# Performance work log

Hardware: AMD Instinct MI355X
Metric: run time of the kernel (lower is better)

## Reference

```python
import jax, jax.numpy as jnp
import numpy as np

B, N, D_MODEL, H, FF = 8, 1024, 1024, 16, 4096
HEAD_DIM = D_MODEL // H
SCALE = float(np.sqrt(HEAD_DIM))


def layer_norm(x, g, b, eps=1e-5):
    mu = jnp.mean(x, axis=-1, keepdims=True)
    var = jnp.var(x, axis=-1, keepdims=True)
    return (x - mu) * jax.lax.rsqrt(var + eps) * g + b


def setup_inputs() -> dict:
    key = jax.random.key(0)
    ks = jax.random.split(key, 16)
    s = lambda fan_in: 1.0 / np.sqrt(fan_in)
    return {
        "hidden_states": jax.random.normal(ks[0], (B, N, D_MODEL), jnp.float32),
        "attention_mask": jnp.zeros((B, N), dtype=bool),
        "qkv_w": jax.random.uniform(ks[1], (3 * D_MODEL, D_MODEL), jnp.float32, -s(D_MODEL), s(D_MODEL)),
        "qkv_b": jnp.zeros((3 * D_MODEL,), jnp.float32),
        "out_w": jax.random.uniform(ks[2], (D_MODEL, D_MODEL), jnp.float32, -s(D_MODEL), s(D_MODEL)),
        "out_b": jnp.zeros((D_MODEL,), jnp.float32),
        "query_weights": jax.random.normal(ks[3], (H, D_MODEL), jnp.float32) * 0.04,  # xavier-ish
        "key_weights": jax.random.normal(ks[4], (H, D_MODEL), jnp.float32) * 0.04,
        "norm1_g": jnp.ones((D_MODEL,), jnp.float32),
        "norm1_b": jnp.zeros((D_MODEL,), jnp.float32),
        "norm2_g": jnp.ones((D_MODEL,), jnp.float32),
        "norm2_b": jnp.zeros((D_MODEL,), jnp.float32),
        "lin1_w": jax.random.uniform(ks[5], (FF, D_MODEL), jnp.float32, -s(D_MODEL), s(D_MODEL)),
        "lin1_b": jnp.zeros((FF,), jnp.float32),
        "lin2_w": jax.random.uniform(ks[6], (D_MODEL, FF // 2), jnp.float32, -s(FF // 2), s(FF // 2)),
        "lin2_b": jnp.zeros((D_MODEL,), jnp.float32),
    }


def reference(hidden_states, attention_mask, qkv_w, qkv_b, out_w, out_b,
              query_weights, key_weights, norm1_g, norm1_b, norm2_g, norm2_b,
              lin1_w, lin1_b, lin2_w, lin2_b):
    b, n, c = hidden_states.shape
    h = layer_norm(hidden_states, norm1_g, norm1_b)
    qkv = (h @ qkv_w.T + qkv_b).reshape(b, n, 3, H, c // H)
    qkv = jnp.transpose(qkv, (2, 0, 3, 1, 4))  # [3, B, H, N, D]
    q, k, v = qkv[0], qkv[1], qkv[2]
    mask4 = attention_mask[:, None, :, None]  # [B,1,N,1]

    # additive attention on keys: per-(head, position) scalar weight, softmax over N
    # (note: original also computes a global_query from q, but it is unused downstream)
    key_attn = k * key_weights[None, :, :, None] / SCALE  # einsum 'bhnd,hn->bhnd'
    key_attn = jnp.where(mask4, -1e9, key_attn)
    key_weight = jax.nn.softmax(key_attn, axis=2)
    global_key = jnp.sum(key_weight * k, axis=2, keepdims=True)  # [B,H,1,D]

    out = v * global_key  # broadcast over N
    out = jnp.transpose(out, (0, 2, 1, 3)).reshape(b, n, c)
    out = out @ out_w.T + out_b
    hidden_states = hidden_states + out

    h2 = layer_norm(hidden_states, norm2_g, norm2_b)
    ff = h2 @ lin1_w.T + lin1_b
    a, g = jnp.split(ff, 2, axis=-1)
    ff = (a * jax.nn.relu(g)) @ lin2_w.T + lin2_b
    return hidden_states + ff
```

## Files before the change

kernel.cpp:

```cpp
#include <hip/hip_runtime.h>
#include <math.h>


#define DM     1024
#define FFH    2048
#define M_TOT  8192

typedef _Float16 f16x8 __attribute__((ext_vector_type(8)));
typedef float    f32x4 __attribute__((ext_vector_type(4)));

__device__ __forceinline__ void gl2lds16(const void* g, void* l) {
    __builtin_amdgcn_global_load_lds(
        (const __attribute__((address_space(1))) void*)g,
        (__attribute__((address_space(3))) void*)l, 16, 0, 0);
}
__device__ __forceinline__ unsigned short f2h(float x) {
    union { _Float16 h; unsigned short u; } c;
    c.h = (_Float16)x;
    return c.u;
}

__global__ __launch_bounds__(256) void wcast_all(
    const float* __restrict__ s0, const float* __restrict__ s1,
    const float* __restrict__ s2, const float* __restrict__ s3,
    unsigned short* __restrict__ d0, unsigned short* __restrict__ d1,
    unsigned short* __restrict__ d2, unsigned short* __restrict__ d3)
{
    const int i = blockIdx.x * 256 + threadIdx.x;
    const float* s; unsigned short* d; int off;
    if      (i <  524288) { s = s0; d = d0; off = i; }
    else if (i <  786432) { s = s1; d = d1; off = i - 524288; }
    else if (i < 1835008) { s = s2; d = d2; off = i - 786432; }
    else                  { s = s3; d = d3; off = i - 1835008; }
    const float4 v = ((const float4*)s)[off];
    ushort4 h;
    h.x = f2h(v.x); h.y = f2h(v.y); h.z = f2h(v.z); h.w = f2h(v.w);
    ((ushort4*)d)[off] = h;
}

__global__ __launch_bounds__(256) void ln_f16(
    const float* __restrict__ x, const float* __restrict__ g,
    const float* __restrict__ b, unsigned short* __restrict__ y)
{
    const int row = blockIdx.x;
    const int t   = threadIdx.x;
    const float4 v = ((const float4*)(x + (size_t)row * DM))[t];

    float s  = v.x + v.y + v.z + v.w;
    float ss = v.x * v.x + v.y * v.y + v.z * v.z + v.w * v.w;
    #pragma unroll
    for (int off = 32; off > 0; off >>= 1) {
        s  += __shfl_xor(s, off);
        ss += __shfl_xor(ss, off);
    }
    __shared__ float sm[8];
    const int wave = t >> 6;
    if ((t & 63) == 0) { sm[wave * 2] = s; sm[wave * 2 + 1] = ss; }
    __syncthreads();
    s  = sm[0] + sm[2] + sm[4] + sm[6];
    ss = sm[1] + sm[3] + sm[5] + sm[7];

    const float mu  = s * (1.0f / DM);
    const float var = ss * (1.0f / DM) - mu * mu;
    const float r   = rsqrtf(var + 1e-5f);

    const float4 gv = ((const float4*)g)[t];
    const float4 bv = ((const float4*)b)[t];
    ushort4 o;
    o.x = f2h((v.x - mu) * r * gv.x + bv.x);
    o.y = f2h((v.y - mu) * r * gv.y + bv.y);
    o.z = f2h((v.z - mu) * r * gv.z + bv.z);
    o.w = f2h((v.w - mu) * r * gv.w + bv.w);
    ((ushort4*)(y + (size_t)row * DM))[t] = o;
}

__global__ __launch_bounds__(256) void attn_kernel(
    const float* __restrict__ kv, const float* __restrict__ kw,
    float* __restrict__ gk)
{
    const int bh = blockIdx.x;
    const int b  = bh >> 4;
    const int h  = bh & 15;
    const int t  = threadIdx.x;
    const int e  = t & 63;
    const int w  = t >> 6;

    const float* kbase = kv + (size_t)b * 1024 * 2048 + h * 64 + e;
    const float* kwr   = kw + h * 1024;

    float m = -1e30f, l = 0.0f, s = 0.0f;
    #pragma unroll 4
    for (int i = 0; i < 256; ++i) {
        const int   n    = (w << 8) + i;
        const float kval = kbase[(size_t)n * 2048];
        const float x    = kval * kwr[n] * 0.125f;
        const float nm   = fmaxf(m, x);
        const float corr = __expf(m - nm);
        const float ex   = __expf(x - nm);
        l = l * corr + ex;
        s = s * corr + ex * kval;
        m = nm;
    }
    __shared__ float sm[3][256];
    sm[0][t] = m; sm[1][t] = l; sm[2][t] = s;
    __syncthreads();
    if (t < 64) {
        #pragma unroll
        for (int ww = 1; ww < 4; ++ww) {
            const float m2 = sm[0][ww * 64 + e];
            const float l2 = sm[1][ww * 64 + e];
            const float s2 = sm[2][ww * 64 + e];
            const float nm = fmaxf(m, m2);
            const float c1 = __expf(m - nm);
            const float c2 = __expf(m2 - nm);
            l = l * c1 + l2 * c2;
            s = s * c1 + s2 * c2;
            m = nm;
        }
        gk[(size_t)b * DM + h * 64 + e] = s / l;
    }
}

__global__ __launch_bounds__(256) void vscale_f16(
    const float* __restrict__ kv, const float* __restrict__ gk,
    unsigned short* __restrict__ vq)
{
    const int m = blockIdx.x;
    const int t = threadIdx.x;
    const int b = m >> 10;
    const float4 v = *(const float4*)(kv + (size_t)m * 2048 + 1024 + t * 4);
    const float4 s = *(const float4*)(gk + b * DM + t * 4);
    ushort4 o;
    o.x = f2h(v.x * s.x);
    o.y = f2h(v.y * s.y);
    o.z = f2h(v.z * s.z);
    o.w = f2h(v.w * s.w);
    *(ushort4*)(vq + (size_t)m * DM + t * 4) = o;
}

template <bool LIN1ACT, bool HAS_RES>
__global__ __launch_bounds__(256) void mfma_gemm(
    const unsigned short* __restrict__ A,
    const unsigned short* __restrict__ B,
    const float* __restrict__ bias,
    const float* __restrict__ residual,
    float* __restrict__ Cf,
    unsigned short* __restrict__ Cq,
    int K, int lda, int ldc)
{
    __shared__ char lds[32768];
    char* ldsA = lds;
    char* ldsB = lds + 16384;

    const int t  = threadIdx.x;
    const int m0 = blockIdx.y * 128;
    const int n0 = blockIdx.x * (LIN1ACT ? 64 : 128);
    const int L  = t & 63;
    const int w  = t >> 6;
    const int wm = w >> 1, wn = w & 1;
    const int fr = L & 15;
    const int q  = L >> 4;

    const unsigned short* Br0 = B + (size_t)n0 * K;
    const unsigned short* Br1 = B + (size_t)(FFH + n0) * K;

    f32x4 acc[4][4];
    #pragma unroll
    for (int i = 0; i < 4; ++i)
        #pragma unroll
        for (int j = 0; j < 4; ++j) acc[i][j] = (f32x4){0.f, 0.f, 0.f, 0.f};

    for (int k0 = 0; k0 < K; k0 += 64) {
        __syncthreads();
        #pragma unroll
        for (int j = 0; j < 4; ++j) {
            const int c   = t + j * 256;
            const int row = c >> 3;
            const int ch  = (c & 7) ^ (row & 7);
            gl2lds16(A + (size_t)(m0 + row) * lda + k0 + ch * 8,
                     ldsA + c * 16);
        }
        #pragma unroll
        for (int j = 0; j < 4; ++j) {
            const int c   = t + j * 256;
            const int row = c >> 3;
            const int ch  = (c & 7) ^ (row & 7);
            const unsigned short* bp = (LIN1ACT && row >= 64) ? Br1 : Br0;
            const int brow = LIN1ACT ? (row & 63) : row;
            gl2lds16(bp + (size_t)brow * K + k0 + ch * 8,
                     ldsB + c * 16);
        }
        __syncthreads();

        #pragma unroll
        for (int s = 0; s < 2; ++s) {
            f16x8 af[4], bf[4];
            #pragma unroll
            for (int mi = 0; mi < 4; ++mi) {
                const int row = wm * 64 + mi * 16 + fr;
                const int ch  = (s * 4 + q) ^ (row & 7);
                af[mi] = *(const f16x8*)(ldsA + row * 128 + ch * 16);
            }
            #pragma unroll
            for (int ni = 0; ni < 4; ++ni) {
                const int row = wn * 64 + ni * 16 + fr;
                const int ch  = (s * 4 + q) ^ (row & 7);
                bf[ni] = *(const f16x8*)(ldsB + row * 128 + ch * 16);
            }
            #pragma unroll
            for (int mi = 0; mi < 4; ++mi)
                #pragma unroll
                for (int ni = 0; ni < 4; ++ni)
                    acc[mi][ni] = __builtin_amdgcn_mfma_f32_16x16x32_f16(
                        af[mi], bf[ni], acc[mi][ni], 0, 0, 0);
        }
    }

    if (!LIN1ACT) {
        float bcol[4];
        #pragma unroll
        for (int ni = 0; ni < 4; ++ni)
            bcol[ni] = bias[n0 + wn * 64 + ni * 16 + fr];
        #pragma unroll
        for (int mi = 0; mi < 4; ++mi)
            #pragma unroll
            for (int ni = 0; ni < 4; ++ni) {
                const int gcol = n0 + wn * 64 + ni * 16 + fr;
                #pragma unroll
                for (int r = 0; r < 4; ++r) {
                    const int grow = m0 + wm * 64 + mi * 16 + q * 4 + r;
                    float v = acc[mi][ni][r] + bcol[ni];
                    if (HAS_RES) v += residual[(size_t)grow * ldc + gcol];
                    Cf[(size_t)grow * ldc + gcol] = v;
                }
            }
    } else {
        __syncthreads();
        float* xch = (float*)lds;
        if (wn == 1) {
            #pragma unroll
            for (int mi = 0; mi < 4; ++mi)
                #pragma unroll
                for (int ni = 0; ni < 4; ++ni) {
                    const int col64 = ni * 16 + fr;
                    const float bg  = bias[FFH + n0 + col64];
                    #pragma unroll
                    for (int r = 0; r < 4; ++r) {
                        const int row64 = mi * 16 + q * 4 + r;
                        xch[wm * 4096 + row64 * 64 + col64] =
                            fmaxf(acc[mi][ni][r] + bg, 0.f);
                    }
                }
        }
        __syncthreads();
        if (wn == 0) {
            #pragma unroll
            for (int mi = 0; mi < 4; ++mi)
                #pragma unroll
                for (int ni = 0; ni < 4; ++ni) {
                    const int col64 = ni * 16 + fr;
                    const float ba  = bias[n0 + col64];
                    #pragma unroll
                    for (int r = 0; r < 4; ++r) {
                        const int row64 = mi * 16 + q * 4 + r;
                        const float a  = acc[mi][ni][r] + ba;
                        const float o  = a * xch[wm * 4096 + row64 * 64 + col64];
                        Cq[(size_t)(m0 + wm * 64 + row64) * FFH + n0 + col64] =
                            f2h(o);
                    }
                }
        }
    }
}

extern "C" void kernel_launch(void* const* d_in, const int* in_sizes, int n_in,
                              void* d_out, int out_size, void* d_ws, size_t ws_size,
                              hipStream_t stream)
{
    const float* hidden = (const float*)d_in[0];
    const float* qkv_w  = (const float*)d_in[2];
    const float* qkv_b  = (const float*)d_in[3];
    const float* out_w  = (const float*)d_in[4];
    const float* out_b  = (const float*)d_in[5];
    const float* key_w  = (const float*)d_in[7];
    const float* n1g    = (const float*)d_in[8];
    const float* n1b    = (const float*)d_in[9];
    const float* n2g    = (const float*)d_in[10];
    const float* n2b    = (const float*)d_in[11];
    const float* l1w    = (const float*)d_in[12];
    const float* l1b    = (const float*)d_in[13];
    const float* l2w    = (const float*)d_in[14];
    const float* l2b    = (const float*)d_in[15];
    float* out = (float*)d_out;
    char*  wsb = (char*)d_ws;

    const size_t MB = 1u << 20;
    unsigned short* h16   = (unsigned short*)wsb;
    float*          kv    = (float*)(wsb + 16 * MB);
    unsigned short* act16 = (unsigned short*)(wsb + 16 * MB);
    unsigned short* vq    = (unsigned short*)(wsb + 80 * MB);
    unsigned short* wkv16 = (unsigned short*)(wsb + 96 * MB);
    unsigned short* wo16  = (unsigned short*)(wsb + 100 * MB);
    unsigned short* wl116 = (unsigned short*)(wsb + 102 * MB);
    unsigned short* wl216 = (unsigned short*)(wsb + 110 * MB);
    float*          gk    = (float*)(wsb + 114 * MB);

    wcast_all<<<9216, 256, 0, stream>>>(
        qkv_w + (size_t)DM * DM, out_w, l1w, l2w,
        wkv16, wo16, wl116, wl216);

    ln_f16<<<M_TOT, 256, 0, stream>>>(hidden, n1g, n1b, h16);

    mfma_gemm<false, false><<<dim3(16, 64), 256, 0, stream>>>(
        h16, wkv16, qkv_b + DM, nullptr, kv, nullptr, 1024, 1024, 2048);

    attn_kernel<<<128, 256, 0, stream>>>(kv, key_w, gk);

    vscale_f16<<<M_TOT, 256, 0, stream>>>(kv, gk, vq);

    mfma_gemm<false, true><<<dim3(8, 64), 256, 0, stream>>>(
        vq, wo16, out_b, hidden, out, nullptr, 1024, 1024, 1024);

    ln_f16<<<M_TOT, 256, 0, stream>>>(out, n2g, n2b, h16);

    mfma_gemm<true, false><<<dim3(32, 64), 256, 0, stream>>>(
        h16, wl116, l1b, nullptr, nullptr, act16, 1024, 1024, 0);

    mfma_gemm<false, true><<<dim3(8, 64), 256, 0, stream>>>(
        act16, wl216, l2b, out, out, nullptr, 2048, 2048, 1024);
}
```

Baseline: 429.8 us.

## Enlarge GEMM tiles, load B from registers, store KV in fp16, split attention

The GEMM is restructured to 256-row tiles with 8x4 MFMA accumulators per wave. Only A goes through LDS; B fragments are loaded straight from global memory into registers and double-buffered across the k-loop. The K/V projection output is now written as fp16 instead of fp32, which halves the traffic into the attention and vscale kernels. The key softmax reduction is split across four times as many blocks plus a small merge kernel to improve parallelism. The trade-offs are higher register pressure (launch bounds 256,2), uncoalesced per-lane B loads from global memory, and fp16 rounding of K/V.

```diff
diff --git a/kernel.cpp b/kernel.cpp
--- a/kernel.cpp
+++ b/kernel.cpp
@@ -18,6 +18,11 @@
     union { _Float16 h; unsigned short u; } c;
     c.h = (_Float16)x;
     return c.u;
+}
+__device__ __forceinline__ float h2f(unsigned short u) {
+    union { unsigned short u; _Float16 h; } c;
+    c.u = u;
+    return (float)c.h;
 }
 
 __global__ __launch_bounds__(256) void wcast_all(
@@ -74,31 +79,29 @@
     ((ushort4*)(y + (size_t)row * DM))[t] = o;
 }
 
-__global__ __launch_bounds__(256) void attn_kernel(
-    const float* __restrict__ kv, const float* __restrict__ kw,
-    float* __restrict__ gk)
-{
-    const int bh = blockIdx.x;
-    const int b  = bh >> 4;
-    const int h  = bh & 15;
-    const int t  = threadIdx.x;
-    const int e  = t & 63;
-    const int w  = t >> 6;
-
-    const float* kbase = kv + (size_t)b * 1024 * 2048 + h * 64 + e;
-    const float* kwr   = kw + h * 1024;
-
-    float m = -1e30f, l = 0.0f, s = 0.0f;
+__global__ __launch_bounds__(256) void attn_part(
+    const unsigned short* __restrict__ kv, const float* __restrict__ kw,
+    float* __restrict__ pm, float* __restrict__ pl, float* __restrict__ ps)
+{
+    const int blk = blockIdx.x;
+    const int bh = blk >> 2, qt = blk & 3;
+    const int b = bh >> 4, h = bh & 15;
+    const int t = threadIdx.x, e = t & 63, w = t >> 6;
+    const int nbase = qt * 256 + w * 64;
+    const unsigned short* kp =
+        kv + (size_t)b * 1024 * 2048 + (size_t)nbase * 2048 + h * 64 + e;
+    const float* kwr = kw + h * 1024 + nbase;
+
+    float m = -1e30f, l = 0.f, s = 0.f;
     #pragma unroll 4
-    for (int i = 0; i < 256; ++i) {
-        const int   n    = (w << 8) + i;
-        const float kval = kbase[(size_t)n * 2048];
-        const float x    = kval * kwr[n] * 0.125f;
+    for (int i = 0; i < 64; ++i) {
+        const float kval = h2f(kp[(size_t)i * 2048]);
+        const float x    = kval * kwr[i] * 0.125f;
         const float nm   = fmaxf(m, x);
-        const float corr = __expf(m - nm);
+        const float c    = __expf(m - nm);
         const float ex   = __expf(x - nm);
-        l = l * corr + ex;
-        s = s * corr + ex * kval;
+        l = l * c + ex;
+        s = s * c + ex * kval;
         m = nm;
     }
     __shared__ float sm[3][256];
@@ -117,156 +120,187 @@
             s = s * c1 + s2 * c2;
             m = nm;
         }
-        gk[(size_t)b * DM + h * 64 + e] = s / l;
-    }
+        const int o = blk * 64 + e;
+        pm[o] = m; pl[o] = l; ps[o] = s;
+    }
+}
+
+__global__ __launch_bounds__(64) void attn_merge(
+    const float* __restrict__ pm, const float* __restrict__ pl,
+    const float* __restrict__ ps, float* __restrict__ gk)
+{
+    const int bh = blockIdx.x, e = threadIdx.x;
+    const int b = bh >> 4, h = bh & 15;
+    int o = bh * 4 * 64 + e;
+    float m = pm[o], l = pl[o], s = ps[o];
+    #pragma unroll
+    for (int qt = 1; qt < 4; ++qt) {
+        o += 64;
+        const float m2 = pm[o], l2 = pl[o], s2 = ps[o];
+        const float nm = fmaxf(m, m2);
+        const float c1 = __expf(m - nm);
+        const float c2 = __expf(m2 - nm);
+        l = l * c1 + l2 * c2;
+        s = s * c1 + s2 * c2;
+        m = nm;
+    }
+    gk[(size_t)b * DM + h * 64 + e] = s / l;
 }
 
 __global__ __launch_bounds__(256) void vscale_f16(
-    const float* __restrict__ kv, const float* __restrict__ gk,
+    const unsigned short* __restrict__ kv, const float* __restrict__ gk,
     unsigned short* __restrict__ vq)
 {
     const int m = blockIdx.x;
     const int t = threadIdx.x;
     const int b = m >> 10;
-    const float4 v = *(const float4*)(kv + (size_t)m * 2048 + 1024 + t * 4);
-    const float4 s = *(const float4*)(gk + b * DM + t * 4);
+    const ushort4 v4 = *(const ushort4*)(kv + (size_t)m * 2048 + 1024 + t * 4);
+    const float4  s4 = *(const float4*)(gk + b * DM + t * 4);
     ushort4 o;
-    o.x = f2h(v.x * s.x);
-    o.y = f2h(v.y * s.y);
-    o.z = f2h(v.z * s.z);
-    o.w = f2h(v.w * s.w);
+    o.x = f2h(h2f(v4.x) * s4.x);
+    o.y = f2h(h2f(v4.y) * s4.y);
+    o.z = f2h(h2f(v4.z) * s4.z);
+    o.w = f2h(h2f(v4.w) * s4.w);
     *(ushort4*)(vq + (size_t)m * DM + t * 4) = o;
 }
 
-template <bool LIN1ACT, bool HAS_RES>
-__global__ __launch_bounds__(256) void mfma_gemm(
+template <bool LIN1ACT, int OUTM>
+__global__ __launch_bounds__(256, 2) void fgemm(
     const unsigned short* __restrict__ A,
     const unsigned short* __restrict__ B,
     const float* __restrict__ bias,
     const float* __restrict__ residual,
-    float* __restrict__ Cf,
-    unsigned short* __restrict__ Cq,
+    float* __restrict__ Cf, unsigned short* __restrict__ Cq,
     int K, int lda, int ldc)
 {
-    __shared__ char lds[32768];
-    char* ldsA = lds;
-    char* ldsB = lds + 16384;
-
+    __shared__ __align__(16) char lds[36864];
     const int t  = threadIdx.x;
-    const int m0 = blockIdx.y * 128;
+    const int m0 = blockIdx.y * 256;
     const int n0 = blockIdx.x * (LIN1ACT ? 64 : 128);
-    const int L  = t & 63;
-    const int w  = t >> 6;
+    const int L  = t & 63, w = t >> 6;
     const int wm = w >> 1, wn = w & 1;
-    const int fr = L & 15;
-    const int q  = L >> 4;
-
-    const unsigned short* Br0 = B + (size_t)n0 * K;
-    const unsigned short* Br1 = B + (size_t)(FFH + n0) * K;
-
-    f32x4 acc[4][4];
-    #pragma unroll
-    for (int i = 0; i < 4; ++i)
+    const int fr = L & 15, q = L >> 4;
+
+    const int arow = t >> 3;
+    const int ach  = (t & 7) ^ (arow & 7);
+    const unsigned short* pA0 = A + (size_t)(m0 + arow) * lda + ach * 8;
+    char* ldsA0 = lds + t * 16;
+
+    const int brow = LIN1ACT ? ((wn ? FFH : 0) + n0 + fr)
+                             : (n0 + wn * 64 + fr);
+    const unsigned short* pB0 = B + (size_t)brow * K + q * 8;
+    const size_t bstep = (size_t)16 * K;
+
+    int aoff[8];
+    #pragma unroll
+    for (int mi = 0; mi < 8; ++mi) {
+        const int row = wm * 128 + mi * 16 + fr;
+        aoff[mi] = row * 128 + ((q ^ (row & 7)) * 16);
+    }
+
+    f32x4 acc[8][4];
+    #pragma unroll
+    for (int i = 0; i < 8; ++i)
         #pragma unroll
         for (int j = 0; j < 4; ++j) acc[i][j] = (f32x4){0.f, 0.f, 0.f, 0.f};
+
+    f16x8 bcur[4];
+    #pragma unroll
+    for (int ni = 0; ni < 4; ++ni)
+        bcur[ni] = *(const f16x8*)(pB0 + ni * bstep);
 
     for (int k0 = 0; k0 < K; k0 += 64) {
         __syncthreads();
         #pragma unroll
-        for (int j = 0; j < 4; ++j) {
-            const int c   = t + j * 256;
-            const int row = c >> 3;
-            const int ch  = (c & 7) ^ (row & 7);
-            gl2lds16(A + (size_t)(m0 + row) * lda + k0 + ch * 8,
-                     ldsA + c * 16);
-        }
-        #pragma unroll
-        for (int j = 0; j < 4; ++j) {
-            const int c   = t + j * 256;
-            const int row = c >> 3;
-            const int ch  = (c & 7) ^ (row & 7);
-            const unsigned short* bp = (LIN1ACT && row >= 64) ? Br1 : Br0;
-            const int brow = LIN1ACT ? (row & 63) : row;
-            gl2lds16(bp + (size_t)brow * K + k0 + ch * 8,
-                     ldsB + c * 16);
-        }
+        for (int j = 0; j < 8; ++j)
+            gl2lds16(pA0 + (size_t)j * 32 * lda + k0, ldsA0 + j * 4096);
+        f16x8 bnxt[4];
+        #pragma unroll
+        for (int ni = 0; ni < 4; ++ni)
+            bnxt[ni] = *(const f16x8*)(pB0 + ni * bstep + k0 + 32);
         __syncthreads();
 
-        #pragma unroll
-        for (int s = 0; s < 2; ++s) {
-            f16x8 af[4], bf[4];
-            #pragma unroll
-            for (int mi = 0; mi < 4; ++mi) {
-                const int row = wm * 64 + mi * 16 + fr;
-                const int ch  = (s * 4 + q) ^ (row & 7);
-                af[mi] = *(const f16x8*)(ldsA + row * 128 + ch * 16);
-            }
-            #pragma unroll
-            for (int ni = 0; ni < 4; ++ni) {
-                const int row = wn * 64 + ni * 16 + fr;
-                const int ch  = (s * 4 + q) ^ (row & 7);
-                bf[ni] = *(const f16x8*)(ldsB + row * 128 + ch * 16);
-            }
-            #pragma unroll
-            for (int mi = 0; mi < 4; ++mi)
-                #pragma unroll
-                for (int ni = 0; ni < 4; ++ni)
-                    acc[mi][ni] = __builtin_amdgcn_mfma_f32_16x16x32_f16(
-                        af[mi], bf[ni], acc[mi][ni], 0, 0, 0);
-        }
+        f16x8 af[8];
+        #pragma unroll
+        for (int mi = 0; mi < 8; ++mi)
+            af[mi] = *(const f16x8*)(lds + aoff[mi]);
+        #pragma unroll
+        for (int mi = 0; mi < 8; ++mi)
+            #pragma unroll
+            for (int ni = 0; ni < 4; ++ni)
+                acc[mi][ni] = __builtin_amdgcn_mfma_f32_16x16x32_f16(
+                    af[mi], bcur[ni], acc[mi][ni], 0, 0, 0);
+
+        const int kn = (k0 + 64 < K) ? (k0 + 64) : 0;
+        #pragma unroll
+        for (int ni = 0; ni < 4; ++ni)
+            bcur[ni] = *(const f16x8*)(pB0 + ni * bstep + kn);
+
+        #pragma unroll
+        for (int mi = 0; mi < 8; ++mi)
+            af[mi] = *(const f16x8*)(lds + (aoff[mi] ^ 64));
+        #pragma unroll
+        for (int mi = 0; mi < 8; ++mi)
+            #pragma unroll
+            for (int ni = 0; ni < 4; ++ni)
+                acc[mi][ni] = __builtin_amdgcn_mfma_f32_16x16x32_f16(
+                    af[mi], bnxt[ni], acc[mi][ni], 0, 0, 0);
     }
 
     if (!LIN1ACT) {
-        float bcol[4];
+        float bc[4];
         #pragma unroll
         for (int ni = 0; ni < 4; ++ni)
-            bcol[ni] = bias[n0 + wn * 64 + ni * 16 + fr];
-        #pragma unroll
-        for (int mi = 0; mi < 4; ++mi)
+            bc[ni] = bias[n0 + wn * 64 + ni * 16 + fr];
+        #pragma unroll
+        for (int mi = 0; mi < 8; ++mi)
             #pragma unroll
             for (int ni = 0; ni < 4; ++ni) {
                 const int gcol = n0 + wn * 64 + ni * 16 + fr;
                 #pragma unroll
                 for (int r = 0; r < 4; ++r) {
-                    const int grow = m0 + wm * 64 + mi * 16 + q * 4 + r;
-                    float v = acc[mi][ni][r] + bcol[ni];
-                    if (HAS_RES) v += residual[(size_t)grow * ldc + gcol];
-                    Cf[(size_t)grow * ldc + gcol] = v;
+                    const int grow = m0 + wm * 128 + mi * 16 + q * 4 + r;
+                    float v = acc[mi][ni][r] + bc[ni];
+                    if (OUTM == 2) {
+                        v += residual[(size_t)grow * ldc + gcol];
+                        Cf[(size_t)grow * ldc + gcol] = v;
+                    } else {
+                        Cq[(size_t)grow * ldc + gcol] = f2h(v);
+                    }
                 }
             }
     } else {
         __syncthreads();
-        float* xch = (float*)lds;
+        unsigned short* xch = (unsigned short*)lds;
         if (wn == 1) {
             #pragma unroll
-            for (int mi = 0; mi < 4; ++mi)
+            for (int mi = 0; mi < 8; ++mi)
                 #pragma unroll
                 for (int ni = 0; ni < 4; ++ni) {
-                    const int col64 = ni * 16 + fr;
-                    const float bg  = bias[FFH + n0 + col64];
+                    const int col = ni * 16 + fr;
+                    const float bg = bias[FFH + n0 + col];
                     #pragma unroll
                     for (int r = 0; r < 4; ++r) {
-                        const int row64 = mi * 16 + q * 4 + r;
-                        xch[wm * 4096 + row64 * 64 + col64] =
-                            fmaxf(acc[mi][ni][r] + bg, 0.f);
+                        const int row = wm * 128 + mi * 16 + q * 4 + r;
+                        xch[row * 72 + col] =
+                            f2h(fmaxf(acc[mi][ni][r] + bg, 0.f));
                     }
                 }
         }
         __syncthreads();
         if (wn == 0) {
             #pragma unroll
-            for (int mi = 0; mi < 4; ++mi)
+            for (int mi = 0; mi < 8; ++mi)
                 #pragma unroll
                 for (int ni = 0; ni < 4; ++ni) {
-                    const int col64 = ni * 16 + fr;
-                    const float ba  = bias[n0 + col64];
+                    const int col = ni * 16 + fr;
+                    const float ba = bias[n0 + col];
                     #pragma unroll
                     for (int r = 0; r < 4; ++r) {
-                        const int row64 = mi * 16 + q * 4 + r;
-                        const float a  = acc[mi][ni][r] + ba;
-                        const float o  = a * xch[wm * 4096 + row64 * 64 + col64];
-                        Cq[(size_t)(m0 + wm * 64 + row64) * FFH + n0 + col64] =
-                            f2h(o);
+                        const int row = wm * 128 + mi * 16 + q * 4 + r;
+                        const float a = acc[mi][ni][r] + ba;
+                        const float o = a * h2f(xch[row * 72 + col]);
+                        Cq[(size_t)(m0 + row) * FFH + n0 + col] = f2h(o);
                     }
                 }
         }
@@ -296,14 +330,17 @@
 
     const size_t MB = 1u << 20;
     unsigned short* h16   = (unsigned short*)wsb;
-    float*          kv    = (float*)(wsb + 16 * MB);
+    unsigned short* kv16  = (unsigned short*)(wsb + 16 * MB);
     unsigned short* act16 = (unsigned short*)(wsb + 16 * MB);
-    unsigned short* vq    = (unsigned short*)(wsb + 80 * MB);
-    unsigned short* wkv16 = (unsigned short*)(wsb + 96 * MB);
-    unsigned short* wo16  = (unsigned short*)(wsb + 100 * MB);
-    unsigned short* wl116 = (unsigned short*)(wsb + 102 * MB);
-    unsigned short* wl216 = (unsigned short*)(wsb + 110 * MB);
-    float*          gk    = (float*)(wsb + 114 * MB);
+    unsigned short* vq    = (unsigned short*)(wsb + 48 * MB);
+    unsigned short* wkv16 = (unsigned short*)(wsb + 64 * MB);
+    unsigned short* wo16  = (unsigned short*)(wsb + 68 * MB);
+    unsigned short* wl116 = (unsigned short*)(wsb + 70 * MB);
+    unsigned short* wl216 = (unsigned short*)(wsb + 78 * MB);
+    float*          gk    = (float*)(wsb + 82 * MB);
+    float*          pm    = (float*)(wsb + 83 * MB);
+    float*          pl    = (float*)(wsb + 83 * MB + 131072);
+    float*          ps    = (float*)(wsb + 83 * MB + 262144);
 
     wcast_all<<<9216, 256, 0, stream>>>(
         qkv_w + (size_t)DM * DM, out_w, l1w, l2w,
@@ -311,21 +348,22 @@
 
     ln_f16<<<M_TOT, 256, 0, stream>>>(hidden, n1g, n1b, h16);
 
-    mfma_gemm<false, false><<<dim3(16, 64), 256, 0, stream>>>(
-        h16, wkv16, qkv_b + DM, nullptr, kv, nullptr, 1024, 1024, 2048);
-
-    attn_kernel<<<128, 256, 0, stream>>>(kv, key_w, gk);
-
-    vscale_f16<<<M_TOT, 256, 0, stream>>>(kv, gk, vq);
-
-    mfma_gemm<false, true><<<dim3(8, 64), 256, 0, stream>>>(
+    fgemm<false, 0><<<dim3(16, 32), 256, 0, stream>>>(
+        h16, wkv16, qkv_b + DM, nullptr, nullptr, kv16, 1024, 1024, 2048);
+
+    attn_part<<<512, 256, 0, stream>>>(kv16, key_w, pm, pl, ps);
+    attn_merge<<<128, 64, 0, stream>>>(pm, pl, ps, gk);
+
+    vscale_f16<<<M_TOT, 256, 0, stream>>>(kv16, gk, vq);
+
+    fgemm<false, 2><<<dim3(8, 32), 256, 0, stream>>>(
         vq, wo16, out_b, hidden, out, nullptr, 1024, 1024, 1024);
 
     ln_f16<<<M_TOT, 256, 0, stream>>>(out, n2g, n2b, h16);
 
-    mfma_gemm<true, false><<<dim3(32, 64), 256, 0, stream>>>(
+    fgemm<true, 0><<<dim3(32, 32), 256, 0, stream>>>(
         h16, wl116, l1b, nullptr, nullptr, act16, 1024, 1024, 0);
 
-    mfma_gemm<false, true><<<dim3(8, 64), 256, 0, stream>>>(
+    fgemm<false, 2><<<dim3(8, 32), 256, 0, stream>>>(
         act16, wl216, l2b, out, out, nullptr, 2048, 2048, 1024);
 }
```

Result: slower. 440.0 us (+2.4%).
